# Performance work log

Hardware: AMD Instinct MI355X
Metric: run time of the kernel (lower is better)

The kernel has to match this reference:

```python
import jax, jax.numpy as jnp
import numpy as np

B, S, D = 4, 2048, 512
H = 8
HD = D // H  # 64


def setup_inputs() -> dict:
    key = jax.random.key(0)
    ks = jax.random.split(key, 11)
    scale = 1.0 / np.sqrt(D)
    inp = {
        "query": jax.random.normal(ks[0], (B, S, D), dtype=jnp.float32),
        "key": jax.random.normal(ks[1], (B, S, D), dtype=jnp.float32),
        "value": jax.random.normal(ks[2], (B, S, D), dtype=jnp.float32),
        "Wq": jax.random.normal(ks[3], (D, D), dtype=jnp.float32) * scale,
        "bq": jnp.zeros((D,), dtype=jnp.float32),
        "Wk": jax.random.normal(ks[4], (D, D), dtype=jnp.float32) * scale,
        "bk": jnp.zeros((D,), dtype=jnp.float32),
        "Wv": jax.random.normal(ks[5], (D, D), dtype=jnp.float32) * scale,
        "bv": jnp.zeros((D,), dtype=jnp.float32),
        "Wo": jax.random.normal(ks[6], (D, D), dtype=jnp.float32) * scale,
        "bo": jnp.zeros((D,), dtype=jnp.float32),
    }
    return inp


def reference(query, key, value, Wq, bq, Wk, bk, Wv, bv, Wo, bo):
    # Linear projections (torch Linear: x @ W.T + b)
    q = (query @ Wq.T + bq).reshape(B, -1, H, HD).transpose(0, 2, 1, 3)  # [B,H,Sq,HD]
    k = (key   @ Wk.T + bk).reshape(B, -1, H, HD).transpose(0, 2, 1, 3)  # [B,H,Sk,HD]
    v = (value @ Wv.T + bv).reshape(B, -1, H, HD).transpose(0, 2, 1, 3)  # [B,H,Sk,HD]

    # Chunked loop in original is mathematically identical to full attention
    scores = jnp.einsum('bhqd,bhkd->bhqk', q, k) / np.sqrt(HD)  # [B,H,Sq,Sk]
    attn = jax.nn.softmax(scores, axis=-1)
    out = jnp.einsum('bhqk,bhkd->bhqd', attn, v)  # [B,H,Sq,HD]
    out = out.transpose(0, 2, 1, 3).reshape(B, -1, D)  # [B,Sq,D]
    return out @ Wo.T + bo
```

## Files before the change

### kernel.cpp

```cpp
#include <hip/hip_runtime.h>
#include <hip/hip_bf16.h>

typedef __attribute__((ext_vector_type(8))) short bf16x8;
typedef __attribute__((ext_vector_type(4))) float f32x4;
typedef __attribute__((ext_vector_type(16))) float f32x16;
typedef __attribute__((ext_vector_type(4))) unsigned int u32x4;

#define MFMA16(a, b, c) __builtin_amdgcn_mfma_f32_16x16x32_bf16((a), (b), (c), 0, 0, 0)
#define MFMA32(a, b, c) __builtin_amdgcn_mfma_f32_32x32x16_bf16((a), (b), (c), 0, 0, 0)

static constexpr int BATCH = 4, S = 2048, DMODEL = 512, H = 8, HD = 64;
static constexpr int M = BATCH * S;

#define WAIT_VM(N) asm volatile("s_waitcnt vmcnt(" #N ")" ::: "memory")
#define WAIT_VM_LGKM(N) asm volatile("s_waitcnt vmcnt(" #N ") lgkmcnt(0)" ::: "memory")
#define SCHEDB() __builtin_amdgcn_sched_barrier(0)

__device__ __forceinline__ float fmax3(float a, float b, float c) {
  return fmaxf(fmaxf(a, b), c);
}

__device__ __forceinline__ float rexp2(float x) {
  float r;
  asm("v_exp_f32 %0, %1" : "=v"(r) : "v"(x));
  return r;
}

__device__ __forceinline__ short f2b(float f) {
  unsigned int u = __builtin_bit_cast(unsigned int, f);
  unsigned int r = (u + 0x7fffu + ((u >> 16) & 1u)) >> 16;
  return (short)r;
}

__device__ __forceinline__ bf16x8 cvt8(const float4& a, const float4& b) {
  bf16x8 r;
  r[0] = f2b(a.x); r[1] = f2b(a.y); r[2] = f2b(a.z); r[3] = f2b(a.w);
  r[4] = f2b(b.x); r[5] = f2b(b.y); r[6] = f2b(b.z); r[7] = f2b(b.w);
  return r;
}

__device__ __forceinline__ void glds16(const void* g, void* l) {
  __builtin_amdgcn_global_load_lds(
      (const __attribute__((address_space(1))) unsigned int*)g,
      (__attribute__((address_space(3))) unsigned int*)l, 16, 0, 0);
}

__global__ __launch_bounds__(256) void convert_w(
    const float* __restrict__ Wq, const float* __restrict__ Wk,
    const float* __restrict__ Wv, const float* __restrict__ Wo,
    short* __restrict__ Wb) {
  const float* src = (blockIdx.y == 0) ? Wq : (blockIdx.y == 1) ? Wk
                   : (blockIdx.y == 2) ? Wv : Wo;
  short* dst = Wb + blockIdx.y * (DMODEL * DMODEL);
  int i = (blockIdx.x * 256 + threadIdx.x) * 8;
  float4 a = *(const float4*)&src[i];
  float4 b = *(const float4*)&src[i + 4];
  *(bf16x8*)&dst[i] = cvt8(a, b);
}

__global__ __launch_bounds__(256) void proj_gemm(
    const float* __restrict__ Aq, const float* __restrict__ Ak, const float* __restrict__ Av,
    const short* __restrict__ Wb,
    const float* __restrict__ bq, const float* __restrict__ bk, const float* __restrict__ bv,
    short* __restrict__ Qp, short* __restrict__ Kp, short* __restrict__ Vp) {
  const int which = blockIdx.y;
  const float* A    = (which == 0) ? Aq : (which == 1) ? Ak : Av;
  const short* W    = Wb + which * (DMODEL * DMODEL);
  const float* bias = (which == 0) ? bq : (which == 1) ? bk : bv;
  short* dst        = (which == 0) ? Qp : (which == 1) ? Kp : Vp;

  const int tm = blockIdx.x & 63;
  const int tn = blockIdx.x >> 6;
  const int m0 = tm * 128, n0 = tn * 128;
  const int t = threadIdx.x;
  const int lane = t & 63, w = t >> 6;
  const int g = lane >> 4, c = lane & 15;
  const int wr = w >> 1, wc = w & 1;

  __shared__ __align__(16) short As[2][128 * 32];
  __shared__ __align__(16) short Bs[3][128 * 32];

  f32x4 acc[4][4];
  const f32x4 fz = {0.f, 0.f, 0.f, 0.f};
#pragma unroll
  for (int i = 0; i < 4; ++i)
#pragma unroll
    for (int j = 0; j < 4; ++j) acc[i][j] = fz;

  const int r0 = t >> 2, c0 = (t & 3) * 8;
  const int r1 = r0 + 64;

  const short* Bsrc0 = W + (n0 + w * 16 + (lane >> 2)) * DMODEL + (lane & 3) * 8;
  const short* Bsrc1 = Bsrc0 + 64 * DMODEL;

  {
    float4 a0 = *(const float4*)&A[(m0 + r0) * DMODEL + c0];
    float4 a1 = *(const float4*)&A[(m0 + r0) * DMODEL + c0 + 4];
    float4 a2 = *(const float4*)&A[(m0 + r1) * DMODEL + c0];
    float4 a3 = *(const float4*)&A[(m0 + r1) * DMODEL + c0 + 4];
    glds16(Bsrc0, &Bs[0][w * 512]);
    glds16(Bsrc1, &Bs[0][2048 + w * 512]);
    glds16(Bsrc0 + 32, &Bs[1][w * 512]);
    glds16(Bsrc1 + 32, &Bs[1][2048 + w * 512]);
    *(bf16x8*)&As[0][r0 * 32 + c0] = cvt8(a0, a1);
    *(bf16x8*)&As[0][r1 * 32 + c0] = cvt8(a2, a3);
  }

  int ob0 = 0, ob1 = 1, ob2 = 2;
  for (int kt = 0; kt < 16; ++kt) {
    if (kt == 15) { WAIT_VM_LGKM(0); } else { WAIT_VM_LGKM(2); }
    __builtin_amdgcn_s_barrier();
    SCHEDB();

    float4 a0, a1, a2, a3;
    if (kt < 15) {
      const int k0 = (kt + 1) * 32;
      a0 = *(const float4*)&A[(m0 + r0) * DMODEL + k0 + c0];
      a1 = *(const float4*)&A[(m0 + r0) * DMODEL + k0 + c0 + 4];
      a2 = *(const float4*)&A[(m0 + r1) * DMODEL + k0 + c0];
      a3 = *(const float4*)&A[(m0 + r1) * DMODEL + k0 + c0 + 4];
    }
    if (kt < 14) {
      const int k0 = (kt + 2) * 32;
      glds16(Bsrc0 + k0, &Bs[ob2][w * 512]);
      glds16(Bsrc1 + k0, &Bs[ob2][2048 + w * 512]);
    }
    SCHEDB();

    bf16x8 af[4], bfr[4];
#pragma unroll
    for (int i = 0; i < 4; ++i)
      af[i] = *(const bf16x8*)&As[kt & 1][(wr * 64 + i * 16 + c) * 32 + g * 8];
#pragma unroll
    for (int j = 0; j < 4; ++j)
      bfr[j] = *(const bf16x8*)&Bs[ob0][(wc * 64 + j * 16 + c) * 32 + g * 8];
    if (which == 2) {
#pragma unroll
      for (int i = 0; i < 4; ++i)
#pragma unroll
        for (int j = 0; j < 4; ++j)
          acc[i][j] = MFMA16(bfr[j], af[i], acc[i][j]);
    } else {
#pragma unroll
      for (int i = 0; i < 4; ++i)
#pragma unroll
        for (int j = 0; j < 4; ++j)
          acc[i][j] = MFMA16(af[i], bfr[j], acc[i][j]);
    }

    if (kt < 15) {
      *(bf16x8*)&As[(kt + 1) & 1][r0 * 32 + c0] = cvt8(a0, a1);
      *(bf16x8*)&As[(kt + 1) & 1][r1 * 32 + c0] = cvt8(a2, a3);
    }
    const int tmp = ob0; ob0 = ob1; ob1 = ob2; ob2 = tmp;
  }

  if (which == 2) {
#pragma unroll
    for (int j = 0; j < 4; ++j) {
#pragma unroll
      for (int r = 0; r < 4; ++r) {
        const int n = n0 + wc * 64 + j * 16 + g * 4 + r;
        const int h = n >> 6, hd = n & 63;
        const float bn = bias[n];
#pragma unroll
        for (int i = 0; i < 4; ++i) {
          const int m = m0 + wr * 64 + i * 16 + c;
          const int bb = m >> 11, s = m & (S - 1);
          dst[((bb * H + h) * HD + hd) * S + s] = f2b(acc[i][j][r] + bn);
        }
      }
    }
  } else {
#pragma unroll
    for (int i = 0; i < 4; ++i) {
#pragma unroll
      for (int j = 0; j < 4; ++j) {
        const int n = n0 + wc * 64 + j * 16 + c;
        const int h = n >> 6, hd = n & 63;
        const float bn = bias[n];
#pragma unroll
        for (int r = 0; r < 4; ++r) {
          const int m = m0 + wr * 64 + i * 16 + g * 4 + r;
          const int bb = m >> 11, s = m & (S - 1);
          dst[((bb * H + h) * S + s) * HD + hd] = f2b(acc[i][j][r] + bn);
        }
      }
    }
  }
}

__global__ __launch_bounds__(256) void out_gemm(
    const short* __restrict__ Am, const short* __restrict__ W,
    const float* __restrict__ bias, float* __restrict__ Out) {
  const int tm = blockIdx.x & 63;
  const int tn = blockIdx.x >> 6;
  const int m0 = tm * 128, n0 = tn * 128;
  const int t = threadIdx.x;
  const int lane = t & 63, w = t >> 6;
  const int g = lane >> 4, c = lane & 15;
  const int wr = w >> 1, wc = w & 1;

  __shared__ __align__(16) short SM[3][2 * 128 * 32];

  f32x4 acc[4][4];
  const f32x4 fz = {0.f, 0.f, 0.f, 0.f};
#pragma unroll
  for (int i = 0; i < 4; ++i)
#pragma unroll
    for (int j = 0; j < 4; ++j) acc[i][j] = fz;

  const short* Asrc0 = Am + (m0 + w * 16 + (lane >> 2)) * DMODEL + (lane & 3) * 8;
  const short* Asrc1 = Asrc0 + 64 * DMODEL;
  const short* Bsrc0 = W + (n0 + w * 16 + (lane >> 2)) * DMODEL + (lane & 3) * 8;
  const short* Bsrc1 = Bsrc0 + 64 * DMODEL;

#pragma unroll
  for (int tt = 0; tt < 2; ++tt) {
    glds16(Asrc0 + tt * 32, &SM[tt][w * 512]);
    glds16(Asrc1 + tt * 32, &SM[tt][2048 + w * 512]);
    glds16(Bsrc0 + tt * 32, &SM[tt][4096 + w * 512]);
    glds16(Bsrc1 + tt * 32, &SM[tt][4096 + 2048 + w * 512]);
  }

  int ob0 = 0, ob1 = 1, ob2 = 2;
  for (int kt = 0; kt < 16; ++kt) {
    if (kt == 15) { WAIT_VM(0); } else { WAIT_VM(4); }
    __builtin_amdgcn_s_barrier();
    SCHEDB();
    if (kt < 14) {
      const int k0 = (kt + 2) * 32;
      glds16(Asrc0 + k0, &SM[ob2][w * 512]);
      glds16(Asrc1 + k0, &SM[ob2][2048 + w * 512]);
      glds16(Bsrc0 + k0, &SM[ob2][4096 + w * 512]);
      glds16(Bsrc1 + k0, &SM[ob2][4096 + 2048 + w * 512]);
    }
    SCHEDB();

    bf16x8 af[4], bfr[4];
#pragma unroll
    for (int i = 0; i < 4; ++i)
      af[i] = *(const bf16x8*)&SM[ob0][(wr * 64 + i * 16 + c) * 32 + g * 8];
#pragma unroll
    for (int j = 0; j < 4; ++j)
      bfr[j] = *(const bf16x8*)&SM[ob0][4096 + (wc * 64 + j * 16 + c) * 32 + g * 8];
#pragma unroll
    for (int i = 0; i < 4; ++i)
#pragma unroll
      for (int j = 0; j < 4; ++j)
        acc[i][j] = MFMA16(af[i], bfr[j], acc[i][j]);

    const int tmp = ob0; ob0 = ob1; ob1 = ob2; ob2 = tmp;
  }

#pragma unroll
  for (int i = 0; i < 4; ++i) {
#pragma unroll
    for (int j = 0; j < 4; ++j) {
      const int n = n0 + wc * 64 + j * 16 + c;
      const float bn = bias[n];
#pragma unroll
      for (int r = 0; r < 4; ++r) {
        const int m = m0 + wr * 64 + i * 16 + g * 4 + r;
        Out[m * DMODEL + n] = acc[i][j][r] + bn;
      }
    }
  }
}

__global__ __launch_bounds__(256, 2) void attn_kernel(
    const short* __restrict__ Qp, const short* __restrict__ Kp,
    const short* __restrict__ VTp, short* __restrict__ att) {
  const int bid = blockIdx.x;
  const int swzb = (bid & 7) * 64 + (bid >> 3);
  const int qt = swzb & 15;
  const int bh = swzb >> 4;
  const int b = bh >> 3, h = bh & 7;
  const short* Q  = Qp  + bh * (S * HD);
  const char*  Kg = (const char*)(Kp  + bh * (S * HD));
  const char*  Vg = (const char*)(VTp + bh * (HD * S));

  const int t = threadIdx.x;
  const int lane = t & 63, w = t >> 6;
  const int l31 = lane & 31, hi = lane >> 5;
  const int q0 = qt * 128 + w * 32;

  __shared__ __align__(16) char smem[3 * 16384];

  const int rowi = lane >> 3;
  const int swzs = ((lane & 7) * 16) ^ (rowi << 4);
  const char* ksrc0 = Kg + (w * 16 + rowi) * 128 + swzs;
  const char* ksrc1 = ksrc0 + 8 * 128;
  const char* vsrc0 = Vg + (w * 16 + rowi) * 4096 + swzs;
  const char* vsrc1 = vsrc0 + 8 * 4096;

  bf16x8 qf[4];
#pragma unroll
  for (int ks = 0; ks < 4; ++ks)
    qf[ks] = *(const bf16x8*)&Q[(q0 + l31) * HD + ks * 16 + hi * 8];

  bf16x8 ones;
#pragma unroll
  for (int i = 0; i < 8; ++i) ones[i] = (short)0x3F80;

  f32x16 o0, o1, osum, fz16;
#pragma unroll
  for (int i = 0; i < 16; ++i) { o0[i] = 0.f; o1[i] = 0.f; osum[i] = 0.f; fz16[i] = 0.f; }
  float mst = -1e30f;

#pragma unroll
  for (int tt = 0; tt < 2; ++tt) {
    char* nb = smem + tt * 16384;
    glds16(ksrc0 + (size_t)tt * 8192, nb + w * 2048);
    glds16(ksrc1 + (size_t)tt * 8192, nb + w * 2048 + 1024);
    glds16(vsrc0 + (size_t)tt * 128, nb + 8192 + w * 2048);
    glds16(vsrc1 + (size_t)tt * 128, nb + 8192 + w * 2048 + 1024);
  }

  const float SCL = 0.18033688011112042f;
  const int fswz = (l31 & 7) << 4;

  int ob0 = 0, ob1 = 16384, ob2 = 32768;
#pragma unroll 2
  for (int kt = 0; kt < 32; ++kt) {
    if (kt == 31) { WAIT_VM(0); } else { WAIT_VM(4); }
    __builtin_amdgcn_s_barrier();
    SCHEDB();
    if (kt < 30) {
      char* nb = smem + ob2;
      const size_t ko = (size_t)(kt + 2) * 8192;
      const size_t vo = (size_t)(kt + 2) * 128;
      glds16(ksrc0 + ko, nb + w * 2048);
      glds16(ksrc1 + ko, nb + w * 2048 + 1024);
      glds16(vsrc0 + vo, nb + 8192 + w * 2048);
      glds16(vsrc1 + vo, nb + 8192 + w * 2048 + 1024);
    }
    SCHEDB();

    const int cb = ob0;
    f32x16 sa0, sa1;
    __builtin_amdgcn_s_setprio(1);
    {
      const int col0 = (hi * 16) ^ fswz;
      const bf16x8 k00 = *(const bf16x8*)&smem[cb + l31 * 128 + col0];
      const bf16x8 k10 = *(const bf16x8*)&smem[cb + (32 + l31) * 128 + col0];
      sa0 = MFMA32(k00, qf[0], fz16);
      sa1 = MFMA32(k10, qf[0], fz16);
    }
#pragma unroll
    for (int ks = 1; ks < 4; ++ks) {
      const int col = (ks * 32 + hi * 16) ^ fswz;
      const bf16x8 k0 = *(const bf16x8*)&smem[cb + l31 * 128 + col];
      const bf16x8 k1 = *(const bf16x8*)&smem[cb + (32 + l31) * 128 + col];
      sa0 = MFMA32(k0, qf[ks], sa0);
      sa1 = MFMA32(k1, qf[ks], sa1);
    }
    __builtin_amdgcn_s_setprio(0);

    float u0 = fmax3(fmax3(sa0[0], sa0[1], sa0[2]), fmax3(sa0[3], sa0[4], sa0[5]),
                     fmax3(sa0[6], sa0[7], sa0[8]));
    float u1 = fmax3(fmax3(sa0[9], sa0[10], sa0[11]), fmax3(sa0[12], sa0[13], sa0[14]),
                     sa0[15]);
    float u2 = fmax3(fmax3(sa1[0], sa1[1], sa1[2]), fmax3(sa1[3], sa1[4], sa1[5]),
                     fmax3(sa1[6], sa1[7], sa1[8]));
    float u3 = fmax3(fmax3(sa1[9], sa1[10], sa1[11]), fmax3(sa1[12], sa1[13], sa1[14]),
                     sa1[15]);
    float mloc = fmax3(fmaxf(u0, u1), u2, u3);
    const float mx = fmaxf(mloc, __shfl_xor(mloc, 32, 64));
    const float mxs = mx * SCL;

    if (!__all(mxs - mst <= 8.0f)) {
      const float mn = fmaxf(mst, mxs);
      const float corr = rexp2(mst - mn);
      osum[0] *= corr;
#pragma unroll
      for (int i = 0; i < 16; ++i) { o0[i] *= corr; o1[i] *= corr; }
      mst = mn;
    }

#pragma unroll
    for (int i = 0; i < 16; ++i) {
      sa0[i] = rexp2(__builtin_fmaf(sa0[i], SCL, -mst));
      sa1[i] = rexp2(__builtin_fmaf(sa1[i], SCL, -mst));
    }

    unsigned int wrd0[8], wrd1[8];
#pragma unroll
    for (int i = 0; i < 8; ++i) {
      asm("v_cvt_pk_bf16_f32 %0, %1, %2" : "=v"(wrd0[i]) : "v"(sa0[2 * i]), "v"(sa0[2 * i + 1]));
      asm("v_cvt_pk_bf16_f32 %0, %1, %2" : "=v"(wrd1[i]) : "v"(sa1[2 * i]), "v"(sa1[2 * i + 1]));
    }

    __builtin_amdgcn_s_setprio(1);
#pragma unroll
    for (int ks = 0; ks < 4; ++ks) {
      const int i0 = (ks & 1) * 4;
      unsigned int a0 = (ks < 2) ? wrd0[i0 + 0] : wrd1[i0 + 0];
      unsigned int b0 = (ks < 2) ? wrd0[i0 + 2] : wrd1[i0 + 2];
      unsigned int a1 = (ks < 2) ? wrd0[i0 + 1] : wrd1[i0 + 1];
      unsigned int b1 = (ks < 2) ? wrd0[i0 + 3] : wrd1[i0 + 3];
      asm("v_permlane32_swap_b32 %0, %1" : "+v"(a0), "+v"(b0));
      asm("v_permlane32_swap_b32 %0, %1" : "+v"(a1), "+v"(b1));
      u32x4 fw;
      fw[0] = a0; fw[1] = a1; fw[2] = b0; fw[3] = b1;
      const bf16x8 pfrag = __builtin_bit_cast(bf16x8, fw);
      const int col = (ks * 32 + hi * 16) ^ fswz;
      const bf16x8 va0 = *(const bf16x8*)&smem[cb + 8192 + l31 * 128 + col];
      const bf16x8 va1 = *(const bf16x8*)&smem[cb + 8192 + (32 + l31) * 128 + col];
      o0 = MFMA32(va0, pfrag, o0);
      o1 = MFMA32(va1, pfrag, o1);
      osum = MFMA32(ones, pfrag, osum);
    }
    __builtin_amdgcn_s_setprio(0);

    const int tmp = ob0; ob0 = ob1; ob1 = ob2; ob2 = tmp;
  }

  const float inv = 1.0f / osum[0];
  short* arow = att + (b * S + q0 + l31) * DMODEL + h * HD;
#pragma unroll
  for (int dt = 0; dt < 2; ++dt) {
#pragma unroll
    for (int rr = 0; rr < 4; ++rr) {
      float v0 = (dt ? o1[4 * rr + 0] : o0[4 * rr + 0]) * inv;
      float v1 = (dt ? o1[4 * rr + 1] : o0[4 * rr + 1]) * inv;
      float v2 = (dt ? o1[4 * rr + 2] : o0[4 * rr + 2]) * inv;
      float v3 = (dt ? o1[4 * rr + 3] : o0[4 * rr + 3]) * inv;
      unsigned int w0, w1;
      asm("v_cvt_pk_bf16_f32 %0, %1, %2" : "=v"(w0) : "v"(v0), "v"(v1));
      asm("v_cvt_pk_bf16_f32 %0, %1, %2" : "=v"(w1) : "v"(v2), "v"(v3));
      uint2 pk2;
      pk2.x = w0; pk2.y = w1;
      *(uint2*)&arow[dt * 32 + rr * 8 + hi * 4] = pk2;
    }
  }
}

extern "C" void kernel_launch(void* const* d_in, const int* in_sizes, int n_in,
                              void* d_out, int out_size, void* d_ws, size_t ws_size,
                              hipStream_t stream) {
  const float* query = (const float*)d_in[0];
  const float* key_  = (const float*)d_in[1];
  const float* value = (const float*)d_in[2];
  const float* Wq = (const float*)d_in[3];
  const float* bq = (const float*)d_in[4];
  const float* Wk = (const float*)d_in[5];
  const float* bk = (const float*)d_in[6];
  const float* Wv = (const float*)d_in[7];
  const float* bv = (const float*)d_in[8];
  const float* Wo = (const float*)d_in[9];
  const float* bo = (const float*)d_in[10];
  float* out = (float*)d_out;

  char* ws = (char*)d_ws;
  const size_t WB_BYTES  = (size_t)4 * DMODEL * DMODEL * 2;
  const size_t MAT_BYTES = (size_t)M * DMODEL * 2;
  short* Wb  = (short*)ws;
  short* Qp  = (short*)(ws + WB_BYTES);
  short* Kp  = (short*)(ws + WB_BYTES + MAT_BYTES);
  short* Vp  = (short*)(ws + WB_BYTES + 2 * MAT_BYTES);
  short* att = (short*)(ws + WB_BYTES + 3 * MAT_BYTES);

  convert_w<<<dim3(128, 4), 256, 0, stream>>>(Wq, Wk, Wv, Wo, Wb);
  proj_gemm<<<dim3(256, 3), 256, 0, stream>>>(query, key_, value, Wb, bq, bk, bv, Qp, Kp, Vp);
  attn_kernel<<<dim3(512), 256, 0, stream>>>(Qp, Kp, Vp, att);
  out_gemm<<<dim3(256), 256, 0, stream>>>(att, Wb + 3 * DMODEL * DMODEL, bo, out);
}
```

Before: 105.9 us.

## Switch attention KV pipeline to 128-key tiles with double buffering

The attention kernel now streams K/V in 128-key tiles with two 32KB shared-memory buffers, instead of 64-key tiles in a triple-buffered ring. Each outer iteration processes two 64-key halves, which halves the number of barriers and loop iterations. Prefetch depth drops from two tiles ahead to one, and the wait is vmcnt(0) every iteration. The aim is lower per-tile synchronisation overhead, at the cost of less latency hiding and a larger LDS footprint, which may reduce occupancy.

```diff
diff --git a/kernel.cpp b/kernel.cpp
--- a/kernel.cpp
+++ b/kernel.cpp
@@ -285,14 +285,16 @@
   const int l31 = lane & 31, hi = lane >> 5;
   const int q0 = qt * 128 + w * 32;
 
-  __shared__ __align__(16) char smem[3 * 16384];
+  __shared__ __align__(16) char smem[2 * 32768];
 
   const int rowi = lane >> 3;
-  const int swzs = ((lane & 7) * 16) ^ (rowi << 4);
-  const char* ksrc0 = Kg + (w * 16 + rowi) * 128 + swzs;
-  const char* ksrc1 = ksrc0 + 8 * 128;
-  const char* vsrc0 = Vg + (w * 16 + rowi) * 4096 + swzs;
-  const char* vsrc1 = vsrc0 + 8 * 4096;
+  const char* ksrc = Kg + (w * 32 + rowi) * 128 + (((lane & 7) * 16) ^ (rowi << 4));
+  const int vrow = lane >> 4;
+  const char* vsrc[4];
+#pragma unroll
+  for (int j = 0; j < 4; ++j)
+    vsrc[j] = Vg + (w * 16 + j * 4 + vrow) * 4096 +
+              (((lane & 15) * 16) ^ (((j * 4 + vrow) & 7) << 4));
 
   bf16x8 qf[4];
 #pragma unroll
@@ -308,112 +310,111 @@
   for (int i = 0; i < 16; ++i) { o0[i] = 0.f; o1[i] = 0.f; osum[i] = 0.f; fz16[i] = 0.f; }
   float mst = -1e30f;
 
-#pragma unroll
-  for (int tt = 0; tt < 2; ++tt) {
-    char* nb = smem + tt * 16384;
-    glds16(ksrc0 + (size_t)tt * 8192, nb + w * 2048);
-    glds16(ksrc1 + (size_t)tt * 8192, nb + w * 2048 + 1024);
-    glds16(vsrc0 + (size_t)tt * 128, nb + 8192 + w * 2048);
-    glds16(vsrc1 + (size_t)tt * 128, nb + 8192 + w * 2048 + 1024);
-  }
-
   const float SCL = 0.18033688011112042f;
   const int fswz = (l31 & 7) << 4;
 
-  int ob0 = 0, ob1 = 16384, ob2 = 32768;
-#pragma unroll 2
-  for (int kt = 0; kt < 32; ++kt) {
-    if (kt == 31) { WAIT_VM(0); } else { WAIT_VM(4); }
+  {
+    char* nb = smem;
+#pragma unroll
+    for (int j = 0; j < 4; ++j) glds16(ksrc + j * 1024, nb + w * 4096 + j * 1024);
+#pragma unroll
+    for (int j = 0; j < 4; ++j) glds16(vsrc[j], nb + 16384 + w * 4096 + j * 1024);
+  }
+
+  for (int kt = 0; kt < 16; ++kt) {
+    WAIT_VM(0);
     __builtin_amdgcn_s_barrier();
     SCHEDB();
-    if (kt < 30) {
-      char* nb = smem + ob2;
-      const size_t ko = (size_t)(kt + 2) * 8192;
-      const size_t vo = (size_t)(kt + 2) * 128;
-      glds16(ksrc0 + ko, nb + w * 2048);
-      glds16(ksrc1 + ko, nb + w * 2048 + 1024);
-      glds16(vsrc0 + vo, nb + 8192 + w * 2048);
-      glds16(vsrc1 + vo, nb + 8192 + w * 2048 + 1024);
-    }
-    SCHEDB();
-
-    const int cb = ob0;
-    f32x16 sa0, sa1;
-    __builtin_amdgcn_s_setprio(1);
-    {
-      const int col0 = (hi * 16) ^ fswz;
-      const bf16x8 k00 = *(const bf16x8*)&smem[cb + l31 * 128 + col0];
-      const bf16x8 k10 = *(const bf16x8*)&smem[cb + (32 + l31) * 128 + col0];
-      sa0 = MFMA32(k00, qf[0], fz16);
-      sa1 = MFMA32(k10, qf[0], fz16);
-    }
-#pragma unroll
-    for (int ks = 1; ks < 4; ++ks) {
-      const int col = (ks * 32 + hi * 16) ^ fswz;
-      const bf16x8 k0 = *(const bf16x8*)&smem[cb + l31 * 128 + col];
-      const bf16x8 k1 = *(const bf16x8*)&smem[cb + (32 + l31) * 128 + col];
-      sa0 = MFMA32(k0, qf[ks], sa0);
-      sa1 = MFMA32(k1, qf[ks], sa1);
-    }
-    __builtin_amdgcn_s_setprio(0);
-
-    float u0 = fmax3(fmax3(sa0[0], sa0[1], sa0[2]), fmax3(sa0[3], sa0[4], sa0[5]),
-                     fmax3(sa0[6], sa0[7], sa0[8]));
-    float u1 = fmax3(fmax3(sa0[9], sa0[10], sa0[11]), fmax3(sa0[12], sa0[13], sa0[14]),
-                     sa0[15]);
-    float u2 = fmax3(fmax3(sa1[0], sa1[1], sa1[2]), fmax3(sa1[3], sa1[4], sa1[5]),
-                     fmax3(sa1[6], sa1[7], sa1[8]));
-    float u3 = fmax3(fmax3(sa1[9], sa1[10], sa1[11]), fmax3(sa1[12], sa1[13], sa1[14]),
-                     sa1[15]);
-    float mloc = fmax3(fmaxf(u0, u1), u2, u3);
-    const float mx = fmaxf(mloc, __shfl_xor(mloc, 32, 64));
-    const float mxs = mx * SCL;
-
-    if (!__all(mxs - mst <= 8.0f)) {
-      const float mn = fmaxf(mst, mxs);
-      const float corr = rexp2(mst - mn);
-      osum[0] *= corr;
-#pragma unroll
-      for (int i = 0; i < 16; ++i) { o0[i] *= corr; o1[i] *= corr; }
-      mst = mn;
-    }
-
-#pragma unroll
-    for (int i = 0; i < 16; ++i) {
-      sa0[i] = rexp2(__builtin_fmaf(sa0[i], SCL, -mst));
-      sa1[i] = rexp2(__builtin_fmaf(sa1[i], SCL, -mst));
-    }
-
-    unsigned int wrd0[8], wrd1[8];
-#pragma unroll
-    for (int i = 0; i < 8; ++i) {
-      asm("v_cvt_pk_bf16_f32 %0, %1, %2" : "=v"(wrd0[i]) : "v"(sa0[2 * i]), "v"(sa0[2 * i + 1]));
-      asm("v_cvt_pk_bf16_f32 %0, %1, %2" : "=v"(wrd1[i]) : "v"(sa1[2 * i]), "v"(sa1[2 * i + 1]));
-    }
-
-    __builtin_amdgcn_s_setprio(1);
-#pragma unroll
-    for (int ks = 0; ks < 4; ++ks) {
-      const int i0 = (ks & 1) * 4;
-      unsigned int a0 = (ks < 2) ? wrd0[i0 + 0] : wrd1[i0 + 0];
-      unsigned int b0 = (ks < 2) ? wrd0[i0 + 2] : wrd1[i0 + 2];
-      unsigned int a1 = (ks < 2) ? wrd0[i0 + 1] : wrd1[i0 + 1];
-      unsigned int b1 = (ks < 2) ? wrd0[i0 + 3] : wrd1[i0 + 3];
-      asm("v_permlane32_swap_b32 %0, %1" : "+v"(a0), "+v"(b0));
-      asm("v_permlane32_swap_b32 %0, %1" : "+v"(a1), "+v"(b1));
-      u32x4 fw;
-      fw[0] = a0; fw[1] = a1; fw[2] = b0; fw[3] = b1;
-      const bf16x8 pfrag = __builtin_bit_cast(bf16x8, fw);
-      const int col = (ks * 32 + hi * 16) ^ fswz;
-      const bf16x8 va0 = *(const bf16x8*)&smem[cb + 8192 + l31 * 128 + col];
-      const bf16x8 va1 = *(const bf16x8*)&smem[cb + 8192 + (32 + l31) * 128 + col];
-      o0 = MFMA32(va0, pfrag, o0);
-      o1 = MFMA32(va1, pfrag, o1);
-      osum = MFMA32(ones, pfrag, osum);
-    }
-    __builtin_amdgcn_s_setprio(0);
-
-    const int tmp = ob0; ob0 = ob1; ob1 = ob2; ob2 = tmp;
+    if (kt < 15) {
+      char* nb = smem + ((kt + 1) & 1) * 32768;
+      const size_t ko = (size_t)(kt + 1) * 16384;
+      const size_t vo = (size_t)(kt + 1) * 256;
+#pragma unroll
+      for (int j = 0; j < 4; ++j) glds16(ksrc + ko + j * 1024, nb + w * 4096 + j * 1024);
+#pragma unroll
+      for (int j = 0; j < 4; ++j) glds16(vsrc[j] + vo, nb + 16384 + w * 4096 + j * 1024);
+    }
+    SCHEDB();
+
+    const int cb = (kt & 1) * 32768;
+#pragma unroll
+    for (int hb = 0; hb < 2; ++hb) {
+      const int kvb = cb + hb * 64 * 128;
+      f32x16 sa0, sa1;
+      __builtin_amdgcn_s_setprio(1);
+      {
+        const int col0 = (hi * 16) ^ fswz;
+        const bf16x8 k00 = *(const bf16x8*)&smem[kvb + l31 * 128 + col0];
+        const bf16x8 k10 = *(const bf16x8*)&smem[kvb + (32 + l31) * 128 + col0];
+        sa0 = MFMA32(k00, qf[0], fz16);
+        sa1 = MFMA32(k10, qf[0], fz16);
+      }
+#pragma unroll
+      for (int ks = 1; ks < 4; ++ks) {
+        const int col = (ks * 32 + hi * 16) ^ fswz;
+        const bf16x8 k0 = *(const bf16x8*)&smem[kvb + l31 * 128 + col];
+        const bf16x8 k1 = *(const bf16x8*)&smem[kvb + (32 + l31) * 128 + col];
+        sa0 = MFMA32(k0, qf[ks], sa0);
+        sa1 = MFMA32(k1, qf[ks], sa1);
+      }
+      __builtin_amdgcn_s_setprio(0);
+
+      float u0 = fmax3(fmax3(sa0[0], sa0[1], sa0[2]), fmax3(sa0[3], sa0[4], sa0[5]),
+                       fmax3(sa0[6], sa0[7], sa0[8]));
+      float u1 = fmax3(fmax3(sa0[9], sa0[10], sa0[11]), fmax3(sa0[12], sa0[13], sa0[14]),
+                       sa0[15]);
+      float u2 = fmax3(fmax3(sa1[0], sa1[1], sa1[2]), fmax3(sa1[3], sa1[4], sa1[5]),
+                       fmax3(sa1[6], sa1[7], sa1[8]));
+      float u3 = fmax3(fmax3(sa1[9], sa1[10], sa1[11]), fmax3(sa1[12], sa1[13], sa1[14]),
+                       sa1[15]);
+      float mloc = fmax3(fmaxf(u0, u1), u2, u3);
+      const float mx = fmaxf(mloc, __shfl_xor(mloc, 32, 64));
+      const float mxs = mx * SCL;
+
+      if (!__all(mxs - mst <= 8.0f)) {
+        const float mn = fmaxf(mst, mxs);
+        const float corr = rexp2(mst - mn);
+        osum[0] *= corr;
+#pragma unroll
+        for (int i = 0; i < 16; ++i) { o0[i] *= corr; o1[i] *= corr; }
+        mst = mn;
+      }
+
+#pragma unroll
+      for (int i = 0; i < 16; ++i) {
+        sa0[i] = rexp2(__builtin_fmaf(sa0[i], SCL, -mst));
+        sa1[i] = rexp2(__builtin_fmaf(sa1[i], SCL, -mst));
+      }
+
+      unsigned int wrd0[8], wrd1[8];
+#pragma unroll
+      for (int i = 0; i < 8; ++i) {
+        asm("v_cvt_pk_bf16_f32 %0, %1, %2" : "=v"(wrd0[i]) : "v"(sa0[2 * i]), "v"(sa0[2 * i + 1]));
+        asm("v_cvt_pk_bf16_f32 %0, %1, %2" : "=v"(wrd1[i]) : "v"(sa1[2 * i]), "v"(sa1[2 * i + 1]));
+      }
+
+      __builtin_amdgcn_s_setprio(1);
+#pragma unroll
+      for (int ks = 0; ks < 4; ++ks) {
+        const int i0 = (ks & 1) * 4;
+        unsigned int a0 = (ks < 2) ? wrd0[i0 + 0] : wrd1[i0 + 0];
+        unsigned int b0 = (ks < 2) ? wrd0[i0 + 2] : wrd1[i0 + 2];
+        unsigned int a1 = (ks < 2) ? wrd0[i0 + 1] : wrd1[i0 + 1];
+        unsigned int b1 = (ks < 2) ? wrd0[i0 + 3] : wrd1[i0 + 3];
+        asm("v_permlane32_swap_b32 %0, %1" : "+v"(a0), "+v"(b0));
+        asm("v_permlane32_swap_b32 %0, %1" : "+v"(a1), "+v"(b1));
+        u32x4 fw;
+        fw[0] = a0; fw[1] = a1; fw[2] = b0; fw[3] = b1;
+        const bf16x8 pfrag = __builtin_bit_cast(bf16x8, fw);
+        const int colv = (hb * 128 + ks * 32 + hi * 16) ^ fswz;
+        const bf16x8 va0 = *(const bf16x8*)&smem[cb + 16384 + l31 * 256 + colv];
+        const bf16x8 va1 = *(const bf16x8*)&smem[cb + 16384 + (32 + l31) * 256 + colv];
+        o0 = MFMA32(va0, pfrag, o0);
+        o1 = MFMA32(va1, pfrag, o1);
+        osum = MFMA32(ones, pfrag, osum);
+      }
+      __builtin_amdgcn_s_setprio(0);
+    }
   }
 
   const float inv = 1.0f / osum[0];
```

After: 106.7 us. About the same (+0.8%).
